# Kernel tuning notes

Hardware: AMD Instinct MI355X
Metric: run time of the kernel (lower is better)

## Reference

```python
import math
import jax, jax.numpy as jnp
import numpy as np

WH, WW = 8, 8
NUM_HEADS = 4
EMBED_DIMS = 128
N_TOK = WH * WW

# --- static relative position index (N, N) ---
_coords = np.stack(np.meshgrid(np.arange(WH), np.arange(WW), indexing='ij')).reshape(2, -1)
_rel = (_coords[:, :, None] - _coords[:, None, :]).transpose(1, 2, 0).copy()
_rel[..., 0] += WH - 1
_rel[..., 1] += WW - 1
_rel[..., 0] *= 2 * WW - 1
REL_INDEX = _rel.sum(-1)  # (N, N) ints in [0, (2Wh-1)(2Ww-1))

# --- static log-spaced relative coords table ((2Wh-1)*(2Ww-1), 2) ---
_ch = np.arange(-(WH - 1), WH, dtype=np.float32)
_cw = np.arange(-(WW - 1), WW, dtype=np.float32)
_tab = np.stack(np.meshgrid(_ch, _cw, indexing='ij')).reshape(2, -1).T.copy()
_tab[:, 0] /= WH - 1
_tab[:, 1] /= WW - 1
_tab *= 8
COORDS_TABLE = np.sign(_tab) * np.log2(np.abs(_tab) + 1.0) / math.log2(8)  # (225, 2)


def setup_inputs() -> dict:
    key = jax.random.key(0)
    ks = jax.random.split(key, 8)
    B_ = 8192
    C = EMBED_DIMS
    H = NUM_HEADS
    return {
        'x': jax.random.normal(ks[0], (B_, N_TOK, C), dtype=jnp.float32),
        'mask': jnp.zeros((256, N_TOK, N_TOK), dtype=jnp.float32),
        'qkv_w': jax.random.normal(ks[1], (3 * C, C), dtype=jnp.float32) * 0.02,
        'q_bias': jnp.zeros((C,), dtype=jnp.float32),
        'v_bias': jnp.zeros((C,), dtype=jnp.float32),
        'logit_scale': jnp.full((H, 1, 1), math.log(10.0), dtype=jnp.float32),
        'cpb_w1': jax.random.normal(ks[2], (512, 2), dtype=jnp.float32) * 0.02,
        'cpb_b1': jnp.zeros((512,), dtype=jnp.float32),
        'cpb_w2': jax.random.normal(ks[3], (H, 512), dtype=jnp.float32) * 0.02,
        'proj_w': jax.random.normal(ks[4], (C, C), dtype=jnp.float32) * 0.02,
        'proj_b': jnp.zeros((C,), dtype=jnp.float32),
    }


def reference(x, mask, qkv_w, q_bias, v_bias, logit_scale, cpb_w1, cpb_b1, cpb_w2, proj_w, proj_b):
    B_, N, C = x.shape
    H = NUM_HEADS
    D = C // H
    # qkv with q/v bias only (k bias is zero)
    qkv_b = jnp.concatenate([q_bias, jnp.zeros_like(v_bias), v_bias])
    qkv = x @ qkv_w.T + qkv_b                           # (B_, N, 3C)
    qkv = qkv.reshape(B_, N, 3, H, D).transpose(2, 0, 3, 1, 4)
    q, k, v = qkv[0], qkv[1], qkv[2]                    # (B_, H, N, D)
    # cosine attention
    qn = q / jnp.clip(jnp.linalg.norm(q, axis=-1, keepdims=True), 1e-12)
    kn = k / jnp.clip(jnp.linalg.norm(k, axis=-1, keepdims=True), 1e-12)
    attn = jnp.einsum('bhnd,bhmd->bhnm', qn, kn)
    scale = jnp.exp(jnp.minimum(logit_scale, math.log(1.0 / 0.01)))  # (H,1,1)
    attn = attn * scale
    # log-CPB relative position bias
    table = jnp.asarray(COORDS_TABLE, dtype=x.dtype)     # (225, 2)
    hdn = jax.nn.relu(table @ cpb_w1.T + cpb_b1)         # (225, 512)
    bias_table = hdn @ cpb_w2.T                          # (225, H)
    rel_idx = jnp.asarray(REL_INDEX.reshape(-1))
    bias = bias_table[rel_idx].reshape(N, N, H).transpose(2, 0, 1)
    bias = 16.0 * jax.nn.sigmoid(bias)                   # (H, N, N)
    attn = attn + bias[None]
    # shifted-window mask
    nW = mask.shape[0]
    attn = attn.reshape(B_ // nW, nW, H, N, N) + mask[None, :, None]
    attn = jax.nn.softmax(attn.reshape(B_, H, N, N), axis=-1)
    out = jnp.einsum('bhnm,bhmd->bhnd', attn, v)
    out = out.transpose(0, 2, 1, 3).reshape(B_, N, C)
    return out @ proj_w.T + proj_b
```

## Files before the change

kernel.cpp:

```cpp
#include <hip/hip_runtime.h>

typedef __attribute__((ext_vector_type(8))) __bf16 bf16x8;
typedef __attribute__((ext_vector_type(4))) float floatx4;

#define WS_BIAS  131072
#define WS_SCALE 196608
#define WS_TBL   196640

static __device__ __forceinline__ unsigned short f2bf_u(float f) {
  union { __bf16 b; unsigned short u; } cv; cv.b = (__bf16)f; return cv.u;
}
static __device__ __forceinline__ unsigned pkbf(float lo, float hi) {
  union { __bf16 b[2]; unsigned u; } cv; cv.b[0] = (__bf16)lo; cv.b[1] = (__bf16)hi; return cv.u;
}

__global__ void k_prep_weights(const float* __restrict__ qkv_w,
                               const float* __restrict__ proj_w,
                               const float* __restrict__ logit_scale,
                               unsigned short* __restrict__ wsQ,
                               float* __restrict__ wsScale)
{
  int t = blockIdx.x * 256 + threadIdx.x;
  int i4 = t * 4;
  float4 v;
  if (i4 < 49152) v = *reinterpret_cast<const float4*>(qkv_w + i4);
  else            v = *reinterpret_cast<const float4*>(proj_w + (i4 - 49152));
  ushort4 pk;
  pk.x = f2bf_u(v.x); pk.y = f2bf_u(v.y); pk.z = f2bf_u(v.z); pk.w = f2bf_u(v.w);
  *reinterpret_cast<ushort4*>(wsQ + i4) = pk;
  if (t < 4) wsScale[t] = expf(fminf(logit_scale[t], 4.6051702f));
}

__global__ void k_cpb_table(const float* __restrict__ w1, const float* __restrict__ b1,
                            const float* __restrict__ w2, float* __restrict__ tbl)
{
  __shared__ float red[256][4];
  int t = blockIdx.x;
  int i = t / 15, j = t % 15;
  float c0 = 8.f * (float)(i - 7) / 7.f;
  float c1 = 8.f * (float)(j - 7) / 7.f;
  c0 = copysignf(log2f(fabsf(c0) + 1.f) / 3.f, c0);
  c1 = copysignf(log2f(fabsf(c1) + 1.f) / 3.f, c1);
  float a0 = 0.f, a1 = 0.f, a2 = 0.f, a3 = 0.f;
  for (int k = threadIdx.x; k < 512; k += 256) {
    float hd = fmaxf(c0 * w1[2*k] + c1 * w1[2*k+1] + b1[k], 0.f);
    a0 += hd * w2[k]; a1 += hd * w2[512+k]; a2 += hd * w2[1024+k]; a3 += hd * w2[1536+k];
  }
  red[threadIdx.x][0]=a0; red[threadIdx.x][1]=a1; red[threadIdx.x][2]=a2; red[threadIdx.x][3]=a3;
  __syncthreads();
  for (int s = 128; s > 0; s >>= 1) {
    if (threadIdx.x < (unsigned)s) {
      red[threadIdx.x][0] += red[threadIdx.x+s][0];
      red[threadIdx.x][1] += red[threadIdx.x+s][1];
      red[threadIdx.x][2] += red[threadIdx.x+s][2];
      red[threadIdx.x][3] += red[threadIdx.x+s][3];
    }
    __syncthreads();
  }
  if (threadIdx.x < 4) tbl[t*4 + threadIdx.x] = red[0][threadIdx.x];
}

__global__ void k_cpb_bias(const float* __restrict__ tbl, float* __restrict__ biasT)
{
  int idx = blockIdx.x * 256 + threadIdx.x;
  int hh = idx >> 12, n = (idx >> 6) & 63, m = idx & 63;
  int rel = ((n >> 3) - (m >> 3) + 7) * 15 + ((n & 7) - (m & 7) + 7);
  float bv = tbl[rel * 4 + hh];
  biasT[idx] = 16.f / (1.f + expf(-bv));
}

__global__ __launch_bounds__(256, 2) void k_wmsa(
    const float* __restrict__ x, const float* __restrict__ mask,
    const unsigned short* __restrict__ wqkv, const unsigned short* __restrict__ wproj,
    const float* __restrict__ q_bias, const float* __restrict__ v_bias,
    const float* __restrict__ biasT, const float* __restrict__ scale4,
    const float* __restrict__ proj_b, float* __restrict__ out)
{
  __shared__ char s_x[64 * 256];
  __shared__ char s_qk[4][8192];
  __shared__ char s_vT[4][4096];

  const int b    = blockIdx.x;
  const int tid  = threadIdx.x;
  const int lane = tid & 63;
  const int h    = tid >> 6;
  const int l15  = lane & 15;
  const int lh   = lane >> 4;
  const int swq  = ((l15 ^ (l15 >> 2)) & 3) << 4;
  const int swp  = (l15 & 7) << 4;
  const floatx4 zf4 = {0.f, 0.f, 0.f, 0.f};

  bf16x8 wvf[4][2], wff[4][4];
  #pragma unroll
  for (int kk = 0; kk < 4; ++kk) {
    #pragma unroll
    for (int ft = 0; ft < 2; ++ft)
      wvf[kk][ft] = *reinterpret_cast<const bf16x8*>(
          wqkv + (size_t)(256 + h * 32 + ft * 16 + l15) * 128 + kk * 32 + lh * 8);
    #pragma unroll
    for (int ff = 0; ff < 4; ++ff) {
      int fb = (ff < 2) ? (h * 32 + ff * 16) : (128 + h * 32 + (ff - 2) * 16);
      wff[kk][ff] = *reinterpret_cast<const bf16x8*>(
          wqkv + (size_t)(fb + l15) * 128 + kk * 32 + lh * 8);
    }
  }
  floatx4 qb0 = *reinterpret_cast<const floatx4*>(q_bias + h * 32 + lh * 4);
  floatx4 qb1 = *reinterpret_cast<const floatx4*>(q_bias + h * 32 + 16 + lh * 4);
  const float vb0 = v_bias[h * 32 + l15], vb1 = v_bias[h * 32 + 16 + l15];
  const float sc  = scale4[h];

  {
    const float* xb = x + (size_t)b * 8192;
    int r = tid >> 2;
    #pragma unroll
    for (int cc = 0; cc < 8; ++cc) {
      int c = (tid & 3) + cc * 4;
      float4 v = reinterpret_cast<const float4*>(xb)[r * 32 + c];
      uint2 w; w.x = pkbf(v.x, v.y); w.y = pkbf(v.z, v.w);
      *reinterpret_cast<uint2*>(s_x + r * 256 + ((c * 8) ^ ((r & 7) << 4))) = w;
    }
  }
  __syncthreads();

  floatx4 vacc[4][2];
  floatx4 qk[4][4];
  #pragma unroll
  for (int mt = 0; mt < 4; ++mt) { vacc[mt][0] = zf4; vacc[mt][1] = zf4; }
  #pragma unroll
  for (int ff = 0; ff < 4; ++ff)
    #pragma unroll
    for (int tt = 0; tt < 4; ++tt) qk[ff][tt] = zf4;

  #pragma unroll
  for (int kk = 0; kk < 4; ++kk) {
    bf16x8 xf[4];
    #pragma unroll
    for (int tt = 0; tt < 4; ++tt) {
      int row = tt * 16 + l15;
      xf[tt] = *reinterpret_cast<const bf16x8*>(
          s_x + row * 256 + (((kk * 32 + lh * 8) * 2) ^ ((row & 7) << 4)));
    }
    #pragma unroll
    for (int ft = 0; ft < 2; ++ft)
      #pragma unroll
      for (int mt = 0; mt < 4; ++mt)
        vacc[mt][ft] = __builtin_amdgcn_mfma_f32_16x16x32_bf16(xf[mt], wvf[kk][ft], vacc[mt][ft], 0, 0, 0);
    #pragma unroll
    for (int ff = 0; ff < 4; ++ff)
      #pragma unroll
      for (int tt = 0; tt < 4; ++tt)
        qk[ff][tt] = __builtin_amdgcn_mfma_f32_16x16x32_bf16(wff[kk][ff], xf[tt], qk[ff][tt], 0, 0, 0);
  }

  {
    char* sv = s_vT[h];
    #pragma unroll
    for (int mt = 0; mt < 4; ++mt) {
      #pragma unroll
      for (int ft = 0; ft < 2; ++ft) {
        float vb = ft ? vb1 : vb0;
        int d = ft * 16 + l15;
        uint2 w;
        w.x = pkbf(vacc[mt][ft][0] + vb, vacc[mt][ft][1] + vb);
        w.y = pkbf(vacc[mt][ft][2] + vb, vacc[mt][ft][3] + vb);
        *reinterpret_cast<uint2*>(sv + d * 128 + (((mt * 16 + lh * 4) * 2) ^ swp)) = w;
      }
    }
  }

  #pragma unroll
  for (int tt = 0; tt < 4; ++tt)
    #pragma unroll
    for (int r = 0; r < 4; ++r) { qk[0][tt][r] += qb0[r]; qk[1][tt][r] += qb1[r]; }
  #pragma unroll
  for (int tt = 0; tt < 4; ++tt) {
    float sq = 0.f, sk = 0.f;
    #pragma unroll
    for (int r = 0; r < 4; ++r) {
      sq += qk[0][tt][r] * qk[0][tt][r] + qk[1][tt][r] * qk[1][tt][r];
      sk += qk[2][tt][r] * qk[2][tt][r] + qk[3][tt][r] * qk[3][tt][r];
    }
    sq += __shfl_xor(sq, 16); sq += __shfl_xor(sq, 32);
    sk += __shfl_xor(sk, 16); sk += __shfl_xor(sk, 32);
    float rq = sc  / fmaxf(sqrtf(sq), 1e-12f);
    float rk = 1.f / fmaxf(sqrtf(sk), 1e-12f);
    #pragma unroll
    for (int r = 0; r < 4; ++r) {
      qk[0][tt][r] *= rq; qk[1][tt][r] *= rq;
      qk[2][tt][r] *= rk; qk[3][tt][r] *= rk;
    }
  }

  floatx4 bb[4][4], mm[4][4];
  {
    const float* bh = biasT + h * 4096;
    const float* mw = mask + (size_t)(b & 255) * 4096;
    #pragma unroll
    for (int tn = 0; tn < 4; ++tn)
      #pragma unroll
      for (int tm = 0; tm < 4; ++tm) {
        int off = (tn * 16 + l15) * 64 + tm * 16 + lh * 4;
        bb[tn][tm] = *reinterpret_cast<const floatx4*>(bh + off);
        mm[tn][tm] = *reinterpret_cast<const floatx4*>(mw + off);
      }
  }

  {
    char* sq = s_qk[h];
    #pragma unroll
    for (int tt = 0; tt < 4; ++tt) {
      int row = 16 * tt + l15;
      #pragma unroll
      for (int ff = 0; ff < 2; ++ff) {
        uint2 wq_, wk_;
        wq_.x = pkbf(qk[ff][tt][0],     qk[ff][tt][1]);
        wq_.y = pkbf(qk[ff][tt][2],     qk[ff][tt][3]);
        wk_.x = pkbf(qk[2 + ff][tt][0], qk[2 + ff][tt][1]);
        wk_.y = pkbf(qk[2 + ff][tt][2], qk[2 + ff][tt][3]);
        int colb = (ff * 32 + lh * 8) ^ swq;
        *reinterpret_cast<uint2*>(sq + row * 64 + colb)        = wq_;
        *reinterpret_cast<uint2*>(sq + 4096 + row * 64 + colb) = wk_;
      }
    }
  }

  floatx4 rs;
  {
    const char* sq = s_qk[h];
    bf16x8 qf[4], kf[4];
    #pragma unroll
    for (int tt = 0; tt < 4; ++tt) {
      int row = 16 * tt + l15;
      qf[tt] = *reinterpret_cast<const bf16x8*>(sq + row * 64 + ((lh * 16) ^ swq));
      kf[tt] = *reinterpret_cast<const bf16x8*>(sq + 4096 + row * 64 + ((lh * 16) ^ swq));
    }
    char* sp = s_qk[h];

    #pragma unroll
    for (int tn = 0; tn < 4; ++tn) {
      floatx4 sacc[4];
      #pragma unroll
      for (int tm = 0; tm < 4; ++tm)
        sacc[tm] = __builtin_amdgcn_mfma_f32_16x16x32_bf16(kf[tm], qf[tn], zf4, 0, 0, 0);
      float sum = 0.f;
      uint2 pw[4];
      #pragma unroll
      for (int tm = 0; tm < 4; ++tm) {
        float e0 = __expf(sacc[tm][0] + bb[tn][tm][0] + mm[tn][tm][0]);
        float e1 = __expf(sacc[tm][1] + bb[tn][tm][1] + mm[tn][tm][1]);
        float e2 = __expf(sacc[tm][2] + bb[tn][tm][2] + mm[tn][tm][2]);
        float e3 = __expf(sacc[tm][3] + bb[tn][tm][3] + mm[tn][tm][3]);
        sum += (e0 + e1) + (e2 + e3);
        pw[tm].x = pkbf(e0, e1); pw[tm].y = pkbf(e2, e3);
      }
      sum += __shfl_xor(sum, 16); sum += __shfl_xor(sum, 32);
      rs[tn] = 1.f / sum;
      int prow = 16 * tn + l15;
      #pragma unroll
      for (int tm = 0; tm < 4; ++tm)
        *reinterpret_cast<uint2*>(sp + prow * 128 + ((tm * 32 + lh * 8) ^ swp)) = pw[tm];
    }
  }

  bf16x8 wp[4][2];
  #pragma unroll
  for (int kk = 0; kk < 4; ++kk)
    #pragma unroll
    for (int ft = 0; ft < 2; ++ft)
      wp[kk][ft] = *reinterpret_cast<const bf16x8*>(
          wproj + (size_t)(h * 32 + ft * 16 + l15) * 128 + kk * 32 + lh * 8);

  floatx4 oacc[2][4];
  #pragma unroll
  for (int dt = 0; dt < 2; ++dt)
    #pragma unroll
    for (int nt = 0; nt < 4; ++nt) oacc[dt][nt] = zf4;
  {
    const char* sv = s_vT[h];
    const char* sp = s_qk[h];
    #pragma unroll
    for (int kk = 0; kk < 2; ++kk) {
      bf16x8 vf[2];
      #pragma unroll
      for (int dt = 0; dt < 2; ++dt)
        vf[dt] = *reinterpret_cast<const bf16x8*>(
            sv + (dt * 16 + l15) * 128 + ((kk * 64 + lh * 16) ^ swp));
      #pragma unroll
      for (int nt = 0; nt < 4; ++nt) {
        bf16x8 pf = *reinterpret_cast<const bf16x8*>(
            sp + (nt * 16 + l15) * 128 + ((kk * 64 + lh * 16) ^ swp));
        #pragma unroll
        for (int dt = 0; dt < 2; ++dt)
          oacc[dt][nt] = __builtin_amdgcn_mfma_f32_16x16x32_bf16(vf[dt], pf, oacc[dt][nt], 0, 0, 0);
      }
    }
  }
  __syncthreads();

  #pragma unroll
  for (int dt = 0; dt < 2; ++dt) {
    #pragma unroll
    for (int nt = 0; nt < 4; ++nt) {
      int n = nt * 16 + l15;
      uint2 w;
      w.x = pkbf(oacc[dt][nt][0] * rs[nt], oacc[dt][nt][1] * rs[nt]);
      w.y = pkbf(oacc[dt][nt][2] * rs[nt], oacc[dt][nt][3] * rs[nt]);
      *reinterpret_cast<uint2*>(
          s_x + n * 256 + (((h * 32 + dt * 16 + lh * 4) * 2) ^ ((n & 7) << 4))) = w;
    }
  }
  __syncthreads();

  floatx4 pacc[4][2];
  #pragma unroll
  for (int mt = 0; mt < 4; ++mt) { pacc[mt][0] = zf4; pacc[mt][1] = zf4; }
  #pragma unroll
  for (int kk = 0; kk < 4; ++kk) {
    bf16x8 of[4];
    #pragma unroll
    for (int mt = 0; mt < 4; ++mt) {
      int row = mt * 16 + l15;
      of[mt] = *reinterpret_cast<const bf16x8*>(
          s_x + row * 256 + (((kk * 32 + lh * 8) * 2) ^ ((row & 7) << 4)));
    }
    #pragma unroll
    for (int ft = 0; ft < 2; ++ft)
      #pragma unroll
      for (int mt = 0; mt < 4; ++mt)
        pacc[mt][ft] = __builtin_amdgcn_mfma_f32_16x16x32_bf16(of[mt], wp[kk][ft], pacc[mt][ft], 0, 0, 0);
  }
  {
    float pb0 = proj_b[h * 32 + l15], pb1 = proj_b[h * 32 + 16 + l15];
    float* ob = out + (size_t)b * 8192;
    #pragma unroll
    for (int mt = 0; mt < 4; ++mt)
      #pragma unroll
      for (int r = 0; r < 4; ++r) {
        int n = mt * 16 + lh * 4 + r;
        ob[n * 128 + h * 32 + l15]      = pacc[mt][0][r] + pb0;
        ob[n * 128 + h * 32 + 16 + l15] = pacc[mt][1][r] + pb1;
      }
  }
}

extern "C" void kernel_launch(void* const* d_in, const int* in_sizes, int n_in,
                              void* d_out, int out_size, void* d_ws, size_t ws_size,
                              hipStream_t stream)
{
  const float* x    = (const float*)d_in[0];
  const float* mask = (const float*)d_in[1];
  const float* qkvw = (const float*)d_in[2];
  const float* qb   = (const float*)d_in[3];
  const float* vb   = (const float*)d_in[4];
  const float* ls   = (const float*)d_in[5];
  const float* w1   = (const float*)d_in[6];
  const float* b1   = (const float*)d_in[7];
  const float* w2   = (const float*)d_in[8];
  const float* pw   = (const float*)d_in[9];
  const float* pb   = (const float*)d_in[10];
  float* out = (float*)d_out;
  char* ws = (char*)d_ws;

  unsigned short* wsQ = (unsigned short*)ws;
  float* wsBias  = (float*)(ws + WS_BIAS);
  float* wsScale = (float*)(ws + WS_SCALE);
  float* wsTbl   = (float*)(ws + WS_TBL);

  hipLaunchKernelGGL(k_prep_weights, dim3(64), dim3(256), 0, stream, qkvw, pw, ls, wsQ, wsScale);
  hipLaunchKernelGGL(k_cpb_table, dim3(225), dim3(256), 0, stream, w1, b1, w2, wsTbl);
  hipLaunchKernelGGL(k_cpb_bias, dim3(64), dim3(256), 0, stream, wsTbl, wsBias);
  hipLaunchKernelGGL(k_wmsa, dim3(8192), dim3(256), 0, stream, x, mask,
                     wsQ, wsQ + 49152, qb, vb, wsBias, wsScale, pb, out);
}
```

Measured before the change: 305.0 us.

## Precompute exp(bias+mask) table and process two windows per block with x prefetch

Adds a kernel that builds a bf16 table of exp(relative bias + mask) for each window/head. The attention kernel then computes exp2(scaled logits) times the table entry, replacing fp32 bias and mask loads plus the add. Each block now handles two windows and prefetches the second window's x into registers while the first is computed, halving the grid. This trades a 4096-block prep kernel, bf16 precision in the bias term, and extra register pressure for less per-window global traffic and some load/compute overlap.

```diff
diff --git a/kernel.cpp b/kernel.cpp
--- a/kernel.cpp
+++ b/kernel.cpp
@@ -6,6 +6,7 @@
 #define WS_BIAS  131072
 #define WS_SCALE 196608
 #define WS_TBL   196640
+#define WS_ETAB  262144
 
 static __device__ __forceinline__ unsigned short f2bf_u(float f) {
   union { __bf16 b; unsigned short u; } cv; cv.b = (__bf16)f; return cv.u;
@@ -13,6 +14,8 @@
 static __device__ __forceinline__ unsigned pkbf(float lo, float hi) {
   union { __bf16 b[2]; unsigned u; } cv; cv.b[0] = (__bf16)lo; cv.b[1] = (__bf16)hi; return cv.u;
 }
+static __device__ __forceinline__ float bfu_lo(unsigned u) { return __uint_as_float(u << 16); }
+static __device__ __forceinline__ float bfu_hi(unsigned u) { return __uint_as_float(u & 0xffff0000u); }
 
 __global__ void k_prep_weights(const float* __restrict__ qkv_w,
                                const float* __restrict__ proj_w,
@@ -69,18 +72,36 @@
   biasT[idx] = 16.f / (1.f + expf(-bv));
 }
 
+__global__ void k_exp_table(const float* __restrict__ biasT, const float* __restrict__ mask,
+                            unsigned short* __restrict__ E)
+{
+  int idx4 = (blockIdx.x * 256 + threadIdx.x) * 4;
+  int wm  = idx4 >> 14;
+  int rem = idx4 & 16383;
+  int hh  = rem >> 12;
+  int nm  = rem & 4095;
+  float4 mv = *reinterpret_cast<const float4*>(mask + (wm << 12) + nm);
+  float4 bv = *reinterpret_cast<const float4*>(biasT + (hh << 12) + nm);
+  ushort4 o;
+  o.x = f2bf_u(expf(bv.x + mv.x));
+  o.y = f2bf_u(expf(bv.y + mv.y));
+  o.z = f2bf_u(expf(bv.z + mv.z));
+  o.w = f2bf_u(expf(bv.w + mv.w));
+  *reinterpret_cast<ushort4*>(E + idx4) = o;
+}
+
 __global__ __launch_bounds__(256, 2) void k_wmsa(
-    const float* __restrict__ x, const float* __restrict__ mask,
+    const float* __restrict__ x,
     const unsigned short* __restrict__ wqkv, const unsigned short* __restrict__ wproj,
     const float* __restrict__ q_bias, const float* __restrict__ v_bias,
-    const float* __restrict__ biasT, const float* __restrict__ scale4,
+    const unsigned short* __restrict__ Etab, const float* __restrict__ scale4,
     const float* __restrict__ proj_b, float* __restrict__ out)
 {
   __shared__ char s_x[64 * 256];
   __shared__ char s_qk[4][8192];
   __shared__ char s_vT[4][4096];
 
-  const int b    = blockIdx.x;
+  const int blk  = blockIdx.x;
   const int tid  = threadIdx.x;
   const int lane = tid & 63;
   const int h    = tid >> 6;
@@ -107,239 +128,262 @@
   floatx4 qb0 = *reinterpret_cast<const floatx4*>(q_bias + h * 32 + lh * 4);
   floatx4 qb1 = *reinterpret_cast<const floatx4*>(q_bias + h * 32 + 16 + lh * 4);
   const float vb0 = v_bias[h * 32 + l15], vb1 = v_bias[h * 32 + 16 + l15];
-  const float sc  = scale4[h];
-
-  {
-    const float* xb = x + (size_t)b * 8192;
-    int r = tid >> 2;
-    #pragma unroll
-    for (int cc = 0; cc < 8; ++cc) {
-      int c = (tid & 3) + cc * 4;
-      float4 v = reinterpret_cast<const float4*>(xb)[r * 32 + c];
-      uint2 w; w.x = pkbf(v.x, v.y); w.y = pkbf(v.z, v.w);
-      *reinterpret_cast<uint2*>(s_x + r * 256 + ((c * 8) ^ ((r & 7) << 4))) = w;
-    }
-  }
-  __syncthreads();
-
-  floatx4 vacc[4][2];
-  floatx4 qk[4][4];
+  const float sc  = scale4[h] * 1.44269504f;
+  const unsigned short* Eh = Etab + ((size_t)((blk & 255) * 4 + h)) * 4096;
+
+  float4 xpre[8];
+
   #pragma unroll
-  for (int mt = 0; mt < 4; ++mt) { vacc[mt][0] = zf4; vacc[mt][1] = zf4; }
-  #pragma unroll
-  for (int ff = 0; ff < 4; ++ff)
-    #pragma unroll
-    for (int tt = 0; tt < 4; ++tt) qk[ff][tt] = zf4;
-
-  #pragma unroll
-  for (int kk = 0; kk < 4; ++kk) {
-    bf16x8 xf[4];
+  for (int wi = 0; wi < 2; ++wi) {
+    const size_t b = (size_t)blk + (size_t)wi * 4096;
+
+    if (wi) __syncthreads();
+
+    {
+      int r = tid >> 2;
+      if (wi == 0) {
+        const float* xb = x + b * 8192;
+        #pragma unroll
+        for (int cc = 0; cc < 8; ++cc) {
+          int c = (tid & 3) + cc * 4;
+          float4 v = reinterpret_cast<const float4*>(xb)[r * 32 + c];
+          uint2 w; w.x = pkbf(v.x, v.y); w.y = pkbf(v.z, v.w);
+          *reinterpret_cast<uint2*>(s_x + r * 256 + ((c * 8) ^ ((r & 7) << 4))) = w;
+        }
+      } else {
+        #pragma unroll
+        for (int cc = 0; cc < 8; ++cc) {
+          int c = (tid & 3) + cc * 4;
+          uint2 w; w.x = pkbf(xpre[cc].x, xpre[cc].y); w.y = pkbf(xpre[cc].z, xpre[cc].w);
+          *reinterpret_cast<uint2*>(s_x + r * 256 + ((c * 8) ^ ((r & 7) << 4))) = w;
+        }
+      }
+    }
+    __syncthreads();
+
+    floatx4 vacc[4][2];
+    floatx4 qk[4][4];
+    #pragma unroll
+    for (int mt = 0; mt < 4; ++mt) { vacc[mt][0] = zf4; vacc[mt][1] = zf4; }
+    #pragma unroll
+    for (int ff = 0; ff < 4; ++ff)
+      #pragma unroll
+      for (int tt = 0; tt < 4; ++tt) qk[ff][tt] = zf4;
+
+    #pragma unroll
+    for (int kk = 0; kk < 4; ++kk) {
+      bf16x8 xf[4];
+      #pragma unroll
+      for (int tt = 0; tt < 4; ++tt) {
+        int row = tt * 16 + l15;
+        xf[tt] = *reinterpret_cast<const bf16x8*>(
+            s_x + row * 256 + (((kk * 32 + lh * 8) * 2) ^ ((row & 7) << 4)));
+      }
+      #pragma unroll
+      for (int ft = 0; ft < 2; ++ft)
+        #pragma unroll
+        for (int mt = 0; mt < 4; ++mt)
+          vacc[mt][ft] = __builtin_amdgcn_mfma_f32_16x16x32_bf16(xf[mt], wvf[kk][ft], vacc[mt][ft], 0, 0, 0);
+      #pragma unroll
+      for (int ff = 0; ff < 4; ++ff)
+        #pragma unroll
+        for (int tt = 0; tt < 4; ++tt)
+          qk[ff][tt] = __builtin_amdgcn_mfma_f32_16x16x32_bf16(wff[kk][ff], xf[tt], qk[ff][tt], 0, 0, 0);
+    }
+
+    {
+      char* sv = s_vT[h];
+      #pragma unroll
+      for (int mt = 0; mt < 4; ++mt) {
+        #pragma unroll
+        for (int ft = 0; ft < 2; ++ft) {
+          float vb = ft ? vb1 : vb0;
+          int d = ft * 16 + l15;
+          uint2 w;
+          w.x = pkbf(vacc[mt][ft][0] + vb, vacc[mt][ft][1] + vb);
+          w.y = pkbf(vacc[mt][ft][2] + vb, vacc[mt][ft][3] + vb);
+          *reinterpret_cast<uint2*>(sv + d * 128 + (((mt * 16 + lh * 4) * 2) ^ swp)) = w;
+        }
+      }
+    }
+
+    #pragma unroll
+    for (int tt = 0; tt < 4; ++tt)
+      #pragma unroll
+      for (int r = 0; r < 4; ++r) { qk[0][tt][r] += qb0[r]; qk[1][tt][r] += qb1[r]; }
     #pragma unroll
     for (int tt = 0; tt < 4; ++tt) {
-      int row = tt * 16 + l15;
-      xf[tt] = *reinterpret_cast<const bf16x8*>(
-          s_x + row * 256 + (((kk * 32 + lh * 8) * 2) ^ ((row & 7) << 4)));
-    }
-    #pragma unroll
-    for (int ft = 0; ft < 2; ++ft)
+      float sq = 0.f, sk = 0.f;
+      #pragma unroll
+      for (int r = 0; r < 4; ++r) {
+        sq += qk[0][tt][r] * qk[0][tt][r] + qk[1][tt][r] * qk[1][tt][r];
+        sk += qk[2][tt][r] * qk[2][tt][r] + qk[3][tt][r] * qk[3][tt][r];
+      }
+      sq += __shfl_xor(sq, 16); sq += __shfl_xor(sq, 32);
+      sk += __shfl_xor(sk, 16); sk += __shfl_xor(sk, 32);
+      float rq = sc  / fmaxf(sqrtf(sq), 1e-12f);
+      float rk = 1.f / fmaxf(sqrtf(sk), 1e-12f);
+      #pragma unroll
+      for (int r = 0; r < 4; ++r) {
+        qk[0][tt][r] *= rq; qk[1][tt][r] *= rq;
+        qk[2][tt][r] *= rk; qk[3][tt][r] *= rk;
+      }
+    }
+
+    uint2 e[4][4];
+    #pragma unroll
+    for (int tn = 0; tn < 4; ++tn)
+      #pragma unroll
+      for (int tm = 0; tm < 4; ++tm)
+        e[tn][tm] = *reinterpret_cast<const uint2*>(
+            Eh + (tn * 16 + l15) * 64 + tm * 16 + lh * 4);
+
+    {
+      char* sq = s_qk[h];
+      #pragma unroll
+      for (int tt = 0; tt < 4; ++tt) {
+        int row = 16 * tt + l15;
+        #pragma unroll
+        for (int ff = 0; ff < 2; ++ff) {
+          uint2 wq_, wk_;
+          wq_.x = pkbf(qk[ff][tt][0],     qk[ff][tt][1]);
+          wq_.y = pkbf(qk[ff][tt][2],     qk[ff][tt][3]);
+          wk_.x = pkbf(qk[2 + ff][tt][0], qk[2 + ff][tt][1]);
+          wk_.y = pkbf(qk[2 + ff][tt][2], qk[2 + ff][tt][3]);
+          int colb = (ff * 32 + lh * 8) ^ swq;
+          *reinterpret_cast<uint2*>(sq + row * 64 + colb)        = wq_;
+          *reinterpret_cast<uint2*>(sq + 4096 + row * 64 + colb) = wk_;
+        }
+      }
+    }
+
+    floatx4 rs;
+    {
+      const char* sq = s_qk[h];
+      bf16x8 qf[4], kf[4];
+      #pragma unroll
+      for (int tt = 0; tt < 4; ++tt) {
+        int row = 16 * tt + l15;
+        qf[tt] = *reinterpret_cast<const bf16x8*>(sq + row * 64 + ((lh * 16) ^ swq));
+        kf[tt] = *reinterpret_cast<const bf16x8*>(sq + 4096 + row * 64 + ((lh * 16) ^ swq));
+      }
+      char* sp = s_qk[h];
+
+      #pragma unroll
+      for (int tn = 0; tn < 4; ++tn) {
+        floatx4 sacc[4];
+        #pragma unroll
+        for (int tm = 0; tm < 4; ++tm)
+          sacc[tm] = __builtin_amdgcn_mfma_f32_16x16x32_bf16(kf[tm], qf[tn], zf4, 0, 0, 0);
+        float sum = 0.f;
+        uint2 pw[4];
+        #pragma unroll
+        for (int tm = 0; tm < 4; ++tm) {
+          uint2 eu = e[tn][tm];
+          float e0 = exp2f(sacc[tm][0]) * bfu_lo(eu.x);
+          float e1 = exp2f(sacc[tm][1]) * bfu_hi(eu.x);
+          float e2 = exp2f(sacc[tm][2]) * bfu_lo(eu.y);
+          float e3 = exp2f(sacc[tm][3]) * bfu_hi(eu.y);
+          sum += (e0 + e1) + (e2 + e3);
+          pw[tm].x = pkbf(e0, e1); pw[tm].y = pkbf(e2, e3);
+        }
+        sum += __shfl_xor(sum, 16); sum += __shfl_xor(sum, 32);
+        rs[tn] = 1.f / sum;
+        int prow = 16 * tn + l15;
+        #pragma unroll
+        for (int tm = 0; tm < 4; ++tm)
+          *reinterpret_cast<uint2*>(sp + prow * 128 + ((tm * 32 + lh * 8) ^ swp)) = pw[tm];
+      }
+    }
+
+    bf16x8 wp[4][2];
+    #pragma unroll
+    for (int kk = 0; kk < 4; ++kk)
+      #pragma unroll
+      for (int ft = 0; ft < 2; ++ft)
+        wp[kk][ft] = *reinterpret_cast<const bf16x8*>(
+            wproj + (size_t)(h * 32 + ft * 16 + l15) * 128 + kk * 32 + lh * 8);
+    if (wi == 0) {
+      const float* xb1 = x + ((size_t)blk + 4096) * 8192;
+      int r = tid >> 2;
+      #pragma unroll
+      for (int cc = 0; cc < 8; ++cc) {
+        int c = (tid & 3) + cc * 4;
+        xpre[cc] = reinterpret_cast<const float4*>(xb1)[r * 32 + c];
+      }
+    }
+
+    floatx4 oacc[2][4];
+    #pragma unroll
+    for (int dt = 0; dt < 2; ++dt)
+      #pragma unroll
+      for (int nt = 0; nt < 4; ++nt) oacc[dt][nt] = zf4;
+    {
+      const char* sv = s_vT[h];
+      const char* sp = s_qk[h];
+      #pragma unroll
+      for (int kk = 0; kk < 2; ++kk) {
+        bf16x8 vf[2];
+        #pragma unroll
+        for (int dt = 0; dt < 2; ++dt)
+          vf[dt] = *reinterpret_cast<const bf16x8*>(
+              sv + (dt * 16 + l15) * 128 + ((kk * 64 + lh * 16) ^ swp));
+        #pragma unroll
+        for (int nt = 0; nt < 4; ++nt) {
+          bf16x8 pf = *reinterpret_cast<const bf16x8*>(
+              sp + (nt * 16 + l15) * 128 + ((kk * 64 + lh * 16) ^ swp));
+          #pragma unroll
+          for (int dt = 0; dt < 2; ++dt)
+            oacc[dt][nt] = __builtin_amdgcn_mfma_f32_16x16x32_bf16(vf[dt], pf, oacc[dt][nt], 0, 0, 0);
+        }
+      }
+    }
+    __syncthreads();
+
+    #pragma unroll
+    for (int dt = 0; dt < 2; ++dt) {
+      #pragma unroll
+      for (int nt = 0; nt < 4; ++nt) {
+        int n = nt * 16 + l15;
+        uint2 w;
+        w.x = pkbf(oacc[dt][nt][0] * rs[nt], oacc[dt][nt][1] * rs[nt]);
+        w.y = pkbf(oacc[dt][nt][2] * rs[nt], oacc[dt][nt][3] * rs[nt]);
+        *reinterpret_cast<uint2*>(
+            s_x + n * 256 + (((h * 32 + dt * 16 + lh * 4) * 2) ^ ((n & 7) << 4))) = w;
+      }
+    }
+    __syncthreads();
+
+    floatx4 pacc[4][2];
+    #pragma unroll
+    for (int mt = 0; mt < 4; ++mt) { pacc[mt][0] = zf4; pacc[mt][1] = zf4; }
+    #pragma unroll
+    for (int kk = 0; kk < 4; ++kk) {
+      bf16x8 of[4];
+      #pragma unroll
+      for (int mt = 0; mt < 4; ++mt) {
+        int row = mt * 16 + l15;
+        of[mt] = *reinterpret_cast<const bf16x8*>(
+            s_x + row * 256 + (((kk * 32 + lh * 8) * 2) ^ ((row & 7) << 4)));
+      }
+      #pragma unroll
+      for (int ft = 0; ft < 2; ++ft)
+        #pragma unroll
+        for (int mt = 0; mt < 4; ++mt)
+          pacc[mt][ft] = __builtin_amdgcn_mfma_f32_16x16x32_bf16(of[mt], wp[kk][ft], pacc[mt][ft], 0, 0, 0);
+    }
+    {
+      float pb0 = proj_b[h * 32 + l15], pb1 = proj_b[h * 32 + 16 + l15];
+      float* ob = out + b * 8192;
       #pragma unroll
       for (int mt = 0; mt < 4; ++mt)
-        vacc[mt][ft] = __builtin_amdgcn_mfma_f32_16x16x32_bf16(xf[mt], wvf[kk][ft], vacc[mt][ft], 0, 0, 0);
-    #pragma unroll
-    for (int ff = 0; ff < 4; ++ff)
-      #pragma unroll
-      for (int tt = 0; tt < 4; ++tt)
-        qk[ff][tt] = __builtin_amdgcn_mfma_f32_16x16x32_bf16(wff[kk][ff], xf[tt], qk[ff][tt], 0, 0, 0);
-  }
-
-  {
-    char* sv = s_vT[h];
-    #pragma unroll
-    for (int mt = 0; mt < 4; ++mt) {
-      #pragma unroll
-      for (int ft = 0; ft < 2; ++ft) {
-        float vb = ft ? vb1 : vb0;
-        int d = ft * 16 + l15;
-        uint2 w;
-        w.x = pkbf(vacc[mt][ft][0] + vb, vacc[mt][ft][1] + vb);
-        w.y = pkbf(vacc[mt][ft][2] + vb, vacc[mt][ft][3] + vb);
-        *reinterpret_cast<uint2*>(sv + d * 128 + (((mt * 16 + lh * 4) * 2) ^ swp)) = w;
-      }
-    }
-  }
-
-  #pragma unroll
-  for (int tt = 0; tt < 4; ++tt)
-    #pragma unroll
-    for (int r = 0; r < 4; ++r) { qk[0][tt][r] += qb0[r]; qk[1][tt][r] += qb1[r]; }
-  #pragma unroll
-  for (int tt = 0; tt < 4; ++tt) {
-    float sq = 0.f, sk = 0.f;
-    #pragma unroll
-    for (int r = 0; r < 4; ++r) {
-      sq += qk[0][tt][r] * qk[0][tt][r] + qk[1][tt][r] * qk[1][tt][r];
-      sk += qk[2][tt][r] * qk[2][tt][r] + qk[3][tt][r] * qk[3][tt][r];
-    }
-    sq += __shfl_xor(sq, 16); sq += __shfl_xor(sq, 32);
-    sk += __shfl_xor(sk, 16); sk += __shfl_xor(sk, 32);
-    float rq = sc  / fmaxf(sqrtf(sq), 1e-12f);
-    float rk = 1.f / fmaxf(sqrtf(sk), 1e-12f);
-    #pragma unroll
-    for (int r = 0; r < 4; ++r) {
-      qk[0][tt][r] *= rq; qk[1][tt][r] *= rq;
-      qk[2][tt][r] *= rk; qk[3][tt][r] *= rk;
-    }
-  }
-
-  floatx4 bb[4][4], mm[4][4];
-  {
-    const float* bh = biasT + h * 4096;
-    const float* mw = mask + (size_t)(b & 255) * 4096;
-    #pragma unroll
-    for (int tn = 0; tn < 4; ++tn)
-      #pragma unroll
-      for (int tm = 0; tm < 4; ++tm) {
-        int off = (tn * 16 + l15) * 64 + tm * 16 + lh * 4;
-        bb[tn][tm] = *reinterpret_cast<const floatx4*>(bh + off);
-        mm[tn][tm] = *reinterpret_cast<const floatx4*>(mw + off);
-      }
-  }
-
-  {
-    char* sq = s_qk[h];
-    #pragma unroll
-    for (int tt = 0; tt < 4; ++tt) {
-      int row = 16 * tt + l15;
-      #pragma unroll
-      for (int ff = 0; ff < 2; ++ff) {
-        uint2 wq_, wk_;
-        wq_.x = pkbf(qk[ff][tt][0],     qk[ff][tt][1]);
-        wq_.y = pkbf(qk[ff][tt][2],     qk[ff][tt][3]);
-        wk_.x = pkbf(qk[2 + ff][tt][0], qk[2 + ff][tt][1]);
-        wk_.y = pkbf(qk[2 + ff][tt][2], qk[2 + ff][tt][3]);
-        int colb = (ff * 32 + lh * 8) ^ swq;
-        *reinterpret_cast<uint2*>(sq + row * 64 + colb)        = wq_;
-        *reinterpret_cast<uint2*>(sq + 4096 + row * 64 + colb) = wk_;
-      }
-    }
-  }
-
-  floatx4 rs;
-  {
-    const char* sq = s_qk[h];
-    bf16x8 qf[4], kf[4];
-    #pragma unroll
-    for (int tt = 0; tt < 4; ++tt) {
-      int row = 16 * tt + l15;
-      qf[tt] = *reinterpret_cast<const bf16x8*>(sq + row * 64 + ((lh * 16) ^ swq));
-      kf[tt] = *reinterpret_cast<const bf16x8*>(sq + 4096 + row * 64 + ((lh * 16) ^ swq));
-    }
-    char* sp = s_qk[h];
-
-    #pragma unroll
-    for (int tn = 0; tn < 4; ++tn) {
-      floatx4 sacc[4];
-      #pragma unroll
-      for (int tm = 0; tm < 4; ++tm)
-        sacc[tm] = __builtin_amdgcn_mfma_f32_16x16x32_bf16(kf[tm], qf[tn], zf4, 0, 0, 0);
-      float sum = 0.f;
-      uint2 pw[4];
-      #pragma unroll
-      for (int tm = 0; tm < 4; ++tm) {
-        float e0 = __expf(sacc[tm][0] + bb[tn][tm][0] + mm[tn][tm][0]);
-        float e1 = __expf(sacc[tm][1] + bb[tn][tm][1] + mm[tn][tm][1]);
-        float e2 = __expf(sacc[tm][2] + bb[tn][tm][2] + mm[tn][tm][2]);
-        float e3 = __expf(sacc[tm][3] + bb[tn][tm][3] + mm[tn][tm][3]);
-        sum += (e0 + e1) + (e2 + e3);
-        pw[tm].x = pkbf(e0, e1); pw[tm].y = pkbf(e2, e3);
-      }
-      sum += __shfl_xor(sum, 16); sum += __shfl_xor(sum, 32);
-      rs[tn] = 1.f / sum;
-      int prow = 16 * tn + l15;
-      #pragma unroll
-      for (int tm = 0; tm < 4; ++tm)
-        *reinterpret_cast<uint2*>(sp + prow * 128 + ((tm * 32 + lh * 8) ^ swp)) = pw[tm];
-    }
-  }
-
-  bf16x8 wp[4][2];
-  #pragma unroll
-  for (int kk = 0; kk < 4; ++kk)
-    #pragma unroll
-    for (int ft = 0; ft < 2; ++ft)
-      wp[kk][ft] = *reinterpret_cast<const bf16x8*>(
-          wproj + (size_t)(h * 32 + ft * 16 + l15) * 128 + kk * 32 + lh * 8);
-
-  floatx4 oacc[2][4];
-  #pragma unroll
-  for (int dt = 0; dt < 2; ++dt)
-    #pragma unroll
-    for (int nt = 0; nt < 4; ++nt) oacc[dt][nt] = zf4;
-  {
-    const char* sv = s_vT[h];
-    const char* sp = s_qk[h];
-    #pragma unroll
-    for (int kk = 0; kk < 2; ++kk) {
-      bf16x8 vf[2];
-      #pragma unroll
-      for (int dt = 0; dt < 2; ++dt)
-        vf[dt] = *reinterpret_cast<const bf16x8*>(
-            sv + (dt * 16 + l15) * 128 + ((kk * 64 + lh * 16) ^ swp));
-      #pragma unroll
-      for (int nt = 0; nt < 4; ++nt) {
-        bf16x8 pf = *reinterpret_cast<const bf16x8*>(
-            sp + (nt * 16 + l15) * 128 + ((kk * 64 + lh * 16) ^ swp));
-        #pragma unroll
-        for (int dt = 0; dt < 2; ++dt)
-          oacc[dt][nt] = __builtin_amdgcn_mfma_f32_16x16x32_bf16(vf[dt], pf, oacc[dt][nt], 0, 0, 0);
-      }
-    }
-  }
-  __syncthreads();
-
-  #pragma unroll
-  for (int dt = 0; dt < 2; ++dt) {
-    #pragma unroll
-    for (int nt = 0; nt < 4; ++nt) {
-      int n = nt * 16 + l15;
-      uint2 w;
-      w.x = pkbf(oacc[dt][nt][0] * rs[nt], oacc[dt][nt][1] * rs[nt]);
-      w.y = pkbf(oacc[dt][nt][2] * rs[nt], oacc[dt][nt][3] * rs[nt]);
-      *reinterpret_cast<uint2*>(
-          s_x + n * 256 + (((h * 32 + dt * 16 + lh * 4) * 2) ^ ((n & 7) << 4))) = w;
-    }
-  }
-  __syncthreads();
-
-  floatx4 pacc[4][2];
-  #pragma unroll
-  for (int mt = 0; mt < 4; ++mt) { pacc[mt][0] = zf4; pacc[mt][1] = zf4; }
-  #pragma unroll
-  for (int kk = 0; kk < 4; ++kk) {
-    bf16x8 of[4];
-    #pragma unroll
-    for (int mt = 0; mt < 4; ++mt) {
-      int row = mt * 16 + l15;
-      of[mt] = *reinterpret_cast<const bf16x8*>(
-          s_x + row * 256 + (((kk * 32 + lh * 8) * 2) ^ ((row & 7) << 4)));
-    }
-    #pragma unroll
-    for (int ft = 0; ft < 2; ++ft)
-      #pragma unroll
-      for (int mt = 0; mt < 4; ++mt)
-        pacc[mt][ft] = __builtin_amdgcn_mfma_f32_16x16x32_bf16(of[mt], wp[kk][ft], pacc[mt][ft], 0, 0, 0);
-  }
-  {
-    float pb0 = proj_b[h * 32 + l15], pb1 = proj_b[h * 32 + 16 + l15];
-    float* ob = out + (size_t)b * 8192;
-    #pragma unroll
-    for (int mt = 0; mt < 4; ++mt)
-      #pragma unroll
-      for (int r = 0; r < 4; ++r) {
-        int n = mt * 16 + lh * 4 + r;
-        ob[n * 128 + h * 32 + l15]      = pacc[mt][0][r] + pb0;
-        ob[n * 128 + h * 32 + 16 + l15] = pacc[mt][1][r] + pb1;
-      }
+        #pragma unroll
+        for (int r = 0; r < 4; ++r) {
+          int n = mt * 16 + lh * 4 + r;
+          ob[n * 128 + h * 32 + l15]      = pacc[mt][0][r] + pb0;
+          ob[n * 128 + h * 32 + 16 + l15] = pacc[mt][1][r] + pb1;
+        }
+    }
   }
 }
 
@@ -365,10 +409,12 @@
   float* wsBias  = (float*)(ws + WS_BIAS);
   float* wsScale = (float*)(ws + WS_SCALE);
   float* wsTbl   = (float*)(ws + WS_TBL);
+  unsigned short* wsE = (unsigned short*)(ws + WS_ETAB);
 
   hipLaunchKernelGGL(k_prep_weights, dim3(64), dim3(256), 0, stream, qkvw, pw, ls, wsQ, wsScale);
   hipLaunchKernelGGL(k_cpb_table, dim3(225), dim3(256), 0, stream, w1, b1, w2, wsTbl);
   hipLaunchKernelGGL(k_cpb_bias, dim3(64), dim3(256), 0, stream, wsTbl, wsBias);
-  hipLaunchKernelGGL(k_wmsa, dim3(8192), dim3(256), 0, stream, x, mask,
-                     wsQ, wsQ + 49152, qb, vb, wsBias, wsScale, pb, out);
-}
+  hipLaunchKernelGGL(k_exp_table, dim3(4096), dim3(256), 0, stream, wsBias, mask, wsE);
+  hipLaunchKernelGGL(k_wmsa, dim3(4096), dim3(256), 0, stream, x,
+                     wsQ, wsQ + 49152, qb, vb, wsE, wsScale, pb, out);
+}
```

Result: faster. 289.6 us (-5.0%).
